# Optimization experiments

Measured on AMD Instinct MI355X. Metric: run time of the kernel, lower is better.

## Reference

```python
import jax, jax.numpy as jnp
import numpy as np

SCALING = 32.0 / 16.0  # alpha / rank

def setup_inputs() -> dict:
    key = jax.random.key(0)
    ks = jax.random.split(key, 6)
    B, S, D_IN, D_OUT, R, N_ADAPT = 32, 1024, 1024, 4096, 16, 8
    hidden_states = jax.random.normal(ks[0], (B, S, D_IN), dtype=jnp.float32)
    adapter_ids = jax.random.randint(ks[1], (B,), 0, N_ADAPT, dtype=jnp.int32)
    W = jax.random.normal(ks[2], (D_IN, D_OUT), dtype=jnp.float32) * 0.02
    bias = jax.random.normal(ks[3], (D_OUT,), dtype=jnp.float32) * 0.02
    lora_a = jax.random.normal(ks[4], (N_ADAPT, D_IN, R), dtype=jnp.float32) * (1.0 / np.sqrt(D_IN))
    lora_b = jax.random.normal(ks[5], (N_ADAPT, R, D_OUT), dtype=jnp.float32) * 0.02
    return {"hidden_states": hidden_states, "adapter_ids": adapter_ids,
            "W": W, "bias": bias, "lora_a": lora_a, "lora_b": lora_b}

def reference(hidden_states, adapter_ids, W, bias, lora_a, lora_b):
    # Base GPT-2 Conv1D: x @ W + b, W: [in, out]
    base_out = jnp.einsum('bsd,do->bso', hidden_states, W) + bias
    # Per-sample routed LoRA: gather each sample's adapter A/B, then batched low-rank matmuls.
    # Equivalent to the torch loop over unique adapter ids with mask/scatter (dropout=0, eval).
    a_sel = lora_a[adapter_ids]  # [B, d_in, r]
    b_sel = lora_b[adapter_ids]  # [B, r, d_out]
    low_rank = jnp.einsum('bsd,bdr->bsr', hidden_states, a_sel)
    delta = jnp.einsum('bsr,bro->bso', low_rank, b_sel) * SCALING
    return base_out + delta
```

## Files before the change

### kernel.cpp

```cpp
#include <hip/hip_runtime.h>
#include <hip/hip_bf16.h>
#include <stdint.h>

constexpr int kB = 32;
constexpr int kS = 1024;
constexpr int kDin = 1024;
constexpr int kDout = 4096;
constexpr int kRank = 16;
constexpr int kNAdapt = 8;
constexpr int kM = kB * kS;
constexpr float kScale = 2.0f;

typedef __attribute__((ext_vector_type(4))) float f32x4;
typedef __attribute__((ext_vector_type(8))) short s16x8;
typedef __attribute__((ext_vector_type(8))) unsigned short u16x8;
typedef __attribute__((ext_vector_type(4))) unsigned short u16x4;

__device__ __forceinline__ unsigned short f2bf(float f) {
  union { float f; uint32_t u; } x; x.f = f;
  uint32_t u = x.u;
  u += 0x7fffu + ((u >> 16) & 1u);
  return (unsigned short)(u >> 16);
}

__global__ void cast_h_kernel(const float* __restrict__ h, unsigned short* __restrict__ out) {
  size_t i = (size_t)blockIdx.x * blockDim.x + threadIdx.x;
  const f32x4* src = reinterpret_cast<const f32x4*>(h) + i * 2;
  f32x4 v0 = src[0], v1 = src[1];
  u16x8 r;
  r[0] = f2bf(v0[0]); r[1] = f2bf(v0[1]); r[2] = f2bf(v0[2]); r[3] = f2bf(v0[3]);
  r[4] = f2bf(v1[0]); r[5] = f2bf(v1[1]); r[6] = f2bf(v1[2]); r[7] = f2bf(v1[3]);
  *reinterpret_cast<u16x8*>(out + i * 8) = r;
}

__global__ __launch_bounds__(256) void build_weff_kernel(
    const float* __restrict__ W,
    const float* __restrict__ la,
    const float* __restrict__ lb,
    unsigned short* __restrict__ weff) {
  __shared__ float Wt[64][68];
  __shared__ float At[64][20];
  __shared__ float Bt[16][68];
  int bid = blockIdx.x;
  int e = bid & 7;
  int rem = bid >> 3;
  int dt = rem >> 6;
  int ot = rem & 63;
  int d0 = dt * 64, o0 = ot * 64;
  int t = threadIdx.x;
  {
    int r = t >> 4;
    int c = (t & 15) * 4;
    const float* wp = W + (size_t)(d0 + r) * kDout + o0 + c;
#pragma unroll
    for (int p = 0; p < 4; ++p) {
      f32x4 v = *reinterpret_cast<const f32x4*>(wp + (size_t)p * 16 * kDout);
      *reinterpret_cast<f32x4*>(&Wt[p * 16 + r][c]) = v;
    }
  }
  {
    int d = t >> 2, r4 = (t & 3) * 4;
    f32x4 v = *reinterpret_cast<const f32x4*>(la + ((size_t)e * kDin + d0 + d) * kRank + r4);
    *reinterpret_cast<f32x4*>(&At[d][r4]) = v;
  }
  {
    int r = t >> 4, c = (t & 15) * 4;
    f32x4 v = *reinterpret_cast<const f32x4*>(lb + ((size_t)e * kRank + r) * kDout + o0 + c);
    *reinterpret_cast<f32x4*>(&Bt[r][c]) = v;
  }
  __syncthreads();
  int ol_base = t >> 4;
  int dl = (t & 15) * 4;
  f32x4 areg[4][4];
#pragma unroll
  for (int j = 0; j < 4; ++j)
#pragma unroll
    for (int q = 0; q < 4; ++q)
      areg[j][q] = *reinterpret_cast<const f32x4*>(&At[dl + j][q * 4]);
#pragma unroll
  for (int p = 0; p < 4; ++p) {
    int ol = p * 16 + ol_base;
    float bv[kRank];
#pragma unroll
    for (int r = 0; r < kRank; ++r) bv[r] = Bt[r][ol];
    u16x4 r4;
#pragma unroll
    for (int j = 0; j < 4; ++j) {
      float acc = 0.f;
#pragma unroll
      for (int q = 0; q < 4; ++q)
        acc += areg[j][q][0] * bv[q * 4 + 0] + areg[j][q][1] * bv[q * 4 + 1] +
               areg[j][q][2] * bv[q * 4 + 2] + areg[j][q][3] * bv[q * 4 + 3];
      r4[j] = f2bf(Wt[dl + j][ol] + kScale * acc);
    }
    *reinterpret_cast<u16x4*>(weff + ((size_t)e * kDout + o0 + ol) * kDin + d0 + dl) = r4;
  }
}

constexpr int BM = 256, BN = 256, BK = 64;
constexpr int MT2 = kM / BM;
constexpr int NT2 = kDout / BN;
constexpr int NWG2 = MT2 * NT2;

__device__ __forceinline__ void gload16(const unsigned short* g, unsigned short* l) {
  __builtin_amdgcn_global_load_lds((const __attribute__((address_space(1))) void*)g,
                                   (__attribute__((address_space(3))) void*)l, 16, 0, 0);
}

#define STG_A3(sa, kk) do { \
  gload16(gA + (size_t)0 * kDin + (kk) * 64, ldst + (sa) * 16384); \
  gload16(gA + (size_t)64 * kDin + (kk) * 64, ldst + (sa) * 16384 + 4096); \
  gload16(gA + (size_t)128 * kDin + (kk) * 64, ldst + (sa) * 16384 + 8192); \
  gload16(gA + (size_t)192 * kDin + (kk) * 64, ldst + (sa) * 16384 + 12288); \
} while (0)
#define STG_B3(sb, kk) do { \
  gload16(gB + (size_t)0 * kDin + (kk) * 64, ldst + 32768 + (sb) * 16384); \
  gload16(gB + (size_t)64 * kDin + (kk) * 64, ldst + 32768 + (sb) * 16384 + 4096); \
  gload16(gB + (size_t)128 * kDin + (kk) * 64, ldst + 32768 + (sb) * 16384 + 8192); \
  gload16(gB + (size_t)192 * kDin + (kk) * 64, ldst + 32768 + (sb) * 16384 + 12288); \
} while (0)

#define RD_A(mh, sa) do { _Pragma("unroll") for (int ii = 0; ii < 4; ++ii) { \
  a[ii][0] = *(const s16x8*)&lds[(sa) * 16384 + aRow + ((mh) * 4 + ii) * 1024 + e0]; \
  a[ii][1] = *(const s16x8*)&lds[(sa) * 16384 + aRow + ((mh) * 4 + ii) * 1024 + e1]; } } while (0)
#define RD_B(nh, breg, sb) do { _Pragma("unroll") for (int jj = 0; jj < 2; ++jj) { \
  breg[jj][0] = *(const s16x8*)&lds[32768 + (sb) * 16384 + bRow + ((nh) * 2 + jj) * 1024 + e0]; \
  breg[jj][1] = *(const s16x8*)&lds[32768 + (sb) * 16384 + bRow + ((nh) * 2 + jj) * 1024 + e1]; } } while (0)

#define MMQ(mh, nh, breg) do { \
  _Pragma("unroll") for (int ii = 0; ii < 4; ++ii) \
  _Pragma("unroll") for (int jj = 0; jj < 2; ++jj) { \
    acc[(mh) * 4 + ii][(nh) * 2 + jj] = __builtin_amdgcn_mfma_f32_16x16x32_bf16( \
        a[ii][0], breg[jj][0], acc[(mh) * 4 + ii][(nh) * 2 + jj], 0, 0, 0); \
    acc[(mh) * 4 + ii][(nh) * 2 + jj] = __builtin_amdgcn_mfma_f32_16x16x32_bf16( \
        a[ii][1], breg[jj][1], acc[(mh) * 4 + ii][(nh) * 2 + jj], 0, 0, 0); } \
} while (0)

#define MM2(mh) do { \
  __builtin_amdgcn_s_setprio(1); \
  MMQ(mh, 0, b0); MMQ(mh, 1, b1); \
  __builtin_amdgcn_s_setprio(0); \
} while (0)

#define BAR1() do { __builtin_amdgcn_sched_barrier(0); __builtin_amdgcn_s_barrier(); \
  asm volatile("s_waitcnt lgkmcnt(0)" ::: "memory"); __builtin_amdgcn_sched_barrier(0); } while (0)
#define BAR2() do { __builtin_amdgcn_sched_barrier(0); __builtin_amdgcn_s_barrier(); } while (0)
#define VMC(n) asm volatile("s_waitcnt vmcnt(" #n ")" ::: "memory")

__global__ __launch_bounds__(512, 2) void gemm256_kernel(
    const unsigned short* __restrict__ Ab,
    const unsigned short* __restrict__ Weff,
    const float* __restrict__ bias,
    const int* __restrict__ aids,
    float* __restrict__ out) {
  __shared__ unsigned short lds[81920];
  int bid = blockIdx.x;
  int swz = (bid & 7) * (NWG2 / 8) + (bid >> 3);
  int mt = swz >> 4, nt = swz & 15;
  int aid = aids[mt >> 2];
  const unsigned short* Aptr = Ab + (size_t)mt * BM * kDin;
  const unsigned short* Bptr = Weff + ((size_t)aid * kDout + (size_t)nt * BN) * kDin;

  int t = threadIdx.x;
  int l = t & 63;
  int w = t >> 6;
  int wm = w >> 2;
  int wn = w & 3;

  int srcColEl = ((t & 7) * 8) ^ (((t >> 3) & 7) << 3);
  const unsigned short* gA = Aptr + (size_t)(t >> 3) * kDin + srcColEl;
  const unsigned short* gB = Bptr + (size_t)(t >> 3) * kDin + srcColEl;
  unsigned short* ldst = lds + t * 8;

  int xmEl = (l & 7) << 3;
  int e0 = (((l >> 4) * 8) ^ xmEl);
  int e1 = e0 ^ 32;
  int aRow = (wm * 128 + (l & 15)) * 64;
  int bRow = (wn * 64 + (l & 15)) * 64;

  f32x4 acc[8][4];
#pragma unroll
  for (int m = 0; m < 8; ++m)
#pragma unroll
    for (int n = 0; n < 4; ++n) acc[m][n] = f32x4{0.f, 0.f, 0.f, 0.f};
  s16x8 a[4][2], b0[2][2], b1[2][2];

  STG_B3(0, 0); STG_A3(0, 0); STG_B3(1, 1);
  VMC(4);
  BAR2();

#pragma unroll
  for (int i = 0; i < 8; ++i) {
    const int kt0 = 2 * i, kt1 = 2 * i + 1;
    const int sb0 = kt0 % 3, sb1 = kt1 % 3;
    const int sb2 = (kt0 + 2) % 3, sb3 = (kt1 + 2) % 3;
    const bool last = (i == 7);
    RD_A(0, 0); RD_B(0, b0, sb0); RD_B(1, b1, sb0);
    STG_A3(1, kt1);
    BAR1(); MM2(0); BAR2();
    RD_A(1, 0);
    if (!last) { STG_B3(sb2, kt0 + 2); VMC(4); } else { VMC(0); }
    BAR1(); MM2(1); BAR2();
    RD_A(0, 1); RD_B(0, b0, sb1); RD_B(1, b1, sb1);
    if (!last) STG_A3(0, kt0 + 2);
    BAR1(); MM2(0); BAR2();
    RD_A(1, 1);
    if (!last) { STG_B3(sb3, kt1 + 2); VMC(4); }
    BAR1(); MM2(1); BAR2();
  }

  size_t row0 = (size_t)mt * BM + wm * 128 + (l >> 4) * 4;
  int col0 = nt * BN + wn * 64 + (l & 15);
#pragma unroll
  for (int nf = 0; nf < 4; ++nf) {
    float bv = bias[col0 + nf * 16];
#pragma unroll
    for (int mf = 0; mf < 8; ++mf) {
#pragma unroll
      for (int j = 0; j < 4; ++j)
        out[(row0 + mf * 16 + j) * kDout + col0 + nf * 16] = acc[mf][nf][j] + bv;
    }
  }
}

extern "C" void kernel_launch(void* const* d_in, const int* in_sizes, int n_in,
                              void* d_out, int out_size, void* d_ws, size_t ws_size,
                              hipStream_t stream) {
  const float* h    = (const float*)d_in[0];
  const int*   aids = (const int*)d_in[1];
  const float* W    = (const float*)d_in[2];
  const float* bias = (const float*)d_in[3];
  const float* la   = (const float*)d_in[4];
  const float* lb   = (const float*)d_in[5];
  float* out = (float*)d_out;

  unsigned short* Abf  = (unsigned short*)d_ws;
  unsigned short* Weff = Abf + (size_t)kM * kDin;

  cast_h_kernel<<<(kM * (size_t)kDin / 8) / 256, 256, 0, stream>>>(h, Abf);
  build_weff_kernel<<<kNAdapt * (kDin / 64) * (kDout / 64), 256, 0, stream>>>(W, la, lb, Weff);
  gemm256_kernel<<<NWG2, 512, 0, stream>>>(Abf, Weff, bias, aids, out);
}
```

Measured before the change: 450.9 us.

## Replace triple-buffered ping-pong GEMM schedule with simple double-buffered k-loop

Restructures the main GEMM loop from a hand-tuned 3-stage B / 2-stage A schedule with setprio and split barriers into a plain double-buffered loop with one barrier pair per k-tile. LDS use drops from 160KB to 128KB per workgroup, and the loads for tile kt+2 are issued after the MFMAs of tile kt finish. This simplifies the schedule and reduces LDS, but it gives up the finer-grained interleaving of loads with compute and the MFMA priority hints. It also adds a full barrier stall each iteration.

```diff
diff --git a/kernel.cpp b/kernel.cpp
--- a/kernel.cpp
+++ b/kernel.cpp
@@ -107,25 +107,25 @@
                                    (__attribute__((address_space(3))) void*)l, 16, 0, 0);
 }
 
-#define STG_A3(sa, kk) do { \
-  gload16(gA + (size_t)0 * kDin + (kk) * 64, ldst + (sa) * 16384); \
-  gload16(gA + (size_t)64 * kDin + (kk) * 64, ldst + (sa) * 16384 + 4096); \
-  gload16(gA + (size_t)128 * kDin + (kk) * 64, ldst + (sa) * 16384 + 8192); \
-  gload16(gA + (size_t)192 * kDin + (kk) * 64, ldst + (sa) * 16384 + 12288); \
+#define STG_A(s, kk) do { \
+  gload16(gA + (size_t)0 * kDin + (kk) * 64, ldst + (s) * 16384); \
+  gload16(gA + (size_t)64 * kDin + (kk) * 64, ldst + (s) * 16384 + 4096); \
+  gload16(gA + (size_t)128 * kDin + (kk) * 64, ldst + (s) * 16384 + 8192); \
+  gload16(gA + (size_t)192 * kDin + (kk) * 64, ldst + (s) * 16384 + 12288); \
 } while (0)
-#define STG_B3(sb, kk) do { \
-  gload16(gB + (size_t)0 * kDin + (kk) * 64, ldst + 32768 + (sb) * 16384); \
-  gload16(gB + (size_t)64 * kDin + (kk) * 64, ldst + 32768 + (sb) * 16384 + 4096); \
-  gload16(gB + (size_t)128 * kDin + (kk) * 64, ldst + 32768 + (sb) * 16384 + 8192); \
-  gload16(gB + (size_t)192 * kDin + (kk) * 64, ldst + 32768 + (sb) * 16384 + 12288); \
+#define STG_B(s, kk) do { \
+  gload16(gB + (size_t)0 * kDin + (kk) * 64, ldst + 32768 + (s) * 16384); \
+  gload16(gB + (size_t)64 * kDin + (kk) * 64, ldst + 32768 + (s) * 16384 + 4096); \
+  gload16(gB + (size_t)128 * kDin + (kk) * 64, ldst + 32768 + (s) * 16384 + 8192); \
+  gload16(gB + (size_t)192 * kDin + (kk) * 64, ldst + 32768 + (s) * 16384 + 12288); \
 } while (0)
 
-#define RD_A(mh, sa) do { _Pragma("unroll") for (int ii = 0; ii < 4; ++ii) { \
-  a[ii][0] = *(const s16x8*)&lds[(sa) * 16384 + aRow + ((mh) * 4 + ii) * 1024 + e0]; \
-  a[ii][1] = *(const s16x8*)&lds[(sa) * 16384 + aRow + ((mh) * 4 + ii) * 1024 + e1]; } } while (0)
-#define RD_B(nh, breg, sb) do { _Pragma("unroll") for (int jj = 0; jj < 2; ++jj) { \
-  breg[jj][0] = *(const s16x8*)&lds[32768 + (sb) * 16384 + bRow + ((nh) * 2 + jj) * 1024 + e0]; \
-  breg[jj][1] = *(const s16x8*)&lds[32768 + (sb) * 16384 + bRow + ((nh) * 2 + jj) * 1024 + e1]; } } while (0)
+#define RD_A(mh, s) do { _Pragma("unroll") for (int ii = 0; ii < 4; ++ii) { \
+  a[ii][0] = *(const s16x8*)&lds[(s) * 16384 + aRow + ((mh) * 4 + ii) * 1024 + e0]; \
+  a[ii][1] = *(const s16x8*)&lds[(s) * 16384 + aRow + ((mh) * 4 + ii) * 1024 + e1]; } } while (0)
+#define RD_B(nh, breg, s) do { _Pragma("unroll") for (int jj = 0; jj < 2; ++jj) { \
+  breg[jj][0] = *(const s16x8*)&lds[32768 + (s) * 16384 + bRow + ((nh) * 2 + jj) * 1024 + e0]; \
+  breg[jj][1] = *(const s16x8*)&lds[32768 + (s) * 16384 + bRow + ((nh) * 2 + jj) * 1024 + e1]; } } while (0)
 
 #define MMQ(mh, nh, breg) do { \
   _Pragma("unroll") for (int ii = 0; ii < 4; ++ii) \
@@ -136,15 +136,6 @@
         a[ii][1], breg[jj][1], acc[(mh) * 4 + ii][(nh) * 2 + jj], 0, 0, 0); } \
 } while (0)
 
-#define MM2(mh) do { \
-  __builtin_amdgcn_s_setprio(1); \
-  MMQ(mh, 0, b0); MMQ(mh, 1, b1); \
-  __builtin_amdgcn_s_setprio(0); \
-} while (0)
-
-#define BAR1() do { __builtin_amdgcn_sched_barrier(0); __builtin_amdgcn_s_barrier(); \
-  asm volatile("s_waitcnt lgkmcnt(0)" ::: "memory"); __builtin_amdgcn_sched_barrier(0); } while (0)
-#define BAR2() do { __builtin_amdgcn_sched_barrier(0); __builtin_amdgcn_s_barrier(); } while (0)
 #define VMC(n) asm volatile("s_waitcnt vmcnt(" #n ")" ::: "memory")
 
 __global__ __launch_bounds__(512, 2) void gemm256_kernel(
@@ -153,7 +144,7 @@
     const float* __restrict__ bias,
     const int* __restrict__ aids,
     float* __restrict__ out) {
-  __shared__ unsigned short lds[81920];
+  __shared__ unsigned short lds[65536];
   int bid = blockIdx.x;
   int swz = (bid & 7) * (NWG2 / 8) + (bid >> 3);
   int mt = swz >> 4, nt = swz & 15;
@@ -185,28 +176,23 @@
     for (int n = 0; n < 4; ++n) acc[m][n] = f32x4{0.f, 0.f, 0.f, 0.f};
   s16x8 a[4][2], b0[2][2], b1[2][2];
 
-  STG_B3(0, 0); STG_A3(0, 0); STG_B3(1, 1);
-  VMC(4);
-  BAR2();
-
-#pragma unroll
-  for (int i = 0; i < 8; ++i) {
-    const int kt0 = 2 * i, kt1 = 2 * i + 1;
-    const int sb0 = kt0 % 3, sb1 = kt1 % 3;
-    const int sb2 = (kt0 + 2) % 3, sb3 = (kt1 + 2) % 3;
-    const bool last = (i == 7);
-    RD_A(0, 0); RD_B(0, b0, sb0); RD_B(1, b1, sb0);
-    STG_A3(1, kt1);
-    BAR1(); MM2(0); BAR2();
-    RD_A(1, 0);
-    if (!last) { STG_B3(sb2, kt0 + 2); VMC(4); } else { VMC(0); }
-    BAR1(); MM2(1); BAR2();
-    RD_A(0, 1); RD_B(0, b0, sb1); RD_B(1, b1, sb1);
-    if (!last) STG_A3(0, kt0 + 2);
-    BAR1(); MM2(0); BAR2();
-    RD_A(1, 1);
-    if (!last) { STG_B3(sb3, kt1 + 2); VMC(4); }
-    BAR1(); MM2(1); BAR2();
+  STG_A(0, 0); STG_B(0, 0);
+  STG_A(1, 1); STG_B(1, 1);
+
+#pragma unroll
+  for (int kt = 0; kt < 16; ++kt) {
+    const int s = kt & 1;
+    if (kt < 15) { VMC(8); } else { VMC(0); }
+    __builtin_amdgcn_s_barrier();
+    __builtin_amdgcn_sched_barrier(0);
+    RD_A(0, s);
+    RD_B(0, b0, s); RD_B(1, b1, s);
+    MMQ(0, 0, b0); MMQ(0, 1, b1);
+    RD_A(1, s);
+    MMQ(1, 0, b0); MMQ(1, 1, b1);
+    __builtin_amdgcn_sched_barrier(0);
+    __builtin_amdgcn_s_barrier();
+    if (kt < 14) { STG_A(s, kt + 2); STG_B(s, kt + 2); }
   }
 
   size_t row0 = (size_t)mt * BM + wm * 128 + (l >> 4) * 4;
```

Result: slower. 480.9 us (+6.7%).
